# Kernel optimization log

Measured on AMD Instinct MI355X. Metric: run time of the kernel, lower is better.

Reference implementation:

```python
import jax, jax.numpy as jnp
import numpy as np

DIM = 4096
B, S = 4, 2048


def setup_inputs() -> dict:
    key = jax.random.key(0)
    ks = jax.random.split(key, 6)
    scale = 1.0 / np.sqrt(DIM)  # nn.Linear-style init scale
    return {
        "x": jax.random.normal(ks[0], (B, S, DIM), dtype=jnp.float32),
        "W1": jax.random.normal(ks[1], (DIM, DIM), dtype=jnp.float32) * scale,
        "W2": jax.random.normal(ks[2], (DIM, DIM), dtype=jnp.float32) * scale,
        "W3": jax.random.normal(ks[3], (DIM, DIM), dtype=jnp.float32) * scale,
        "W4": jax.random.normal(ks[4], (DIM, DIM), dtype=jnp.float32) * scale,
        "Wo": jax.random.normal(ks[5], (DIM, DIM), dtype=jnp.float32) * scale,
    }


def reference(x, W1, W2, W3, W4, Wo):
    # nn.Linear(bias=False): y = x @ W.T
    xA = jnp.einsum('bsd,ed->bse', x, W1)
    xB = jnp.einsum('bsd,ed->bse', x, W2)
    xC = jnp.einsum('bsd,ed->bse', x, W3)
    # xA^T @ xB over the sequence axis -> [B, dim, dim]
    sq = jnp.einsum('bsd,bse->bde', xA, xB)
    sq = jax.nn.softmax(sq, axis=-1)
    # xC @ sq -> [B, S, dim]
    xO = jnp.einsum('bsd,bde->bse', xC, sq)
    xO = jax.nn.softmax(xO, axis=-1)
    xO = jax.nn.silu(jnp.einsum('bsd,ed->bse', xO, W4))
    return jnp.einsum('bsd,ed->bse', x + xO, Wo)
```

## Files before the change

kernel.cpp:

```cpp
#include <hip/hip_runtime.h>
#include <hip/hip_bf16.h>
#include <stdint.h>

#define DIM 4096
#define NB 4
#define SEQ 2048

typedef __bf16 bf16_t;
typedef __bf16 bf16x8 __attribute__((ext_vector_type(8)));
typedef float f32x4 __attribute__((ext_vector_type(4)));

__device__ __forceinline__ uint16_t f2bf_u(float f) {
  union { float f; uint32_t u; } v; v.f = f;
  uint32_t r = v.u + 0x7FFFu + ((v.u >> 16) & 1u);
  return (uint16_t)(r >> 16);
}

__global__ __launch_bounds__(256) void cvt_f32_bf16_k(const float* __restrict__ in,
                                                      uint16_t* __restrict__ out, long n) {
  long i = ((long)blockIdx.x * 256 + threadIdx.x) * 8;
  long stride = (long)gridDim.x * 256 * 8;
  for (; i < n; i += stride) {
    float4 a = *(const float4*)(in + i);
    float4 b = *(const float4*)(in + i + 4);
    ushort4 o0 = make_ushort4(f2bf_u(a.x), f2bf_u(a.y), f2bf_u(a.z), f2bf_u(a.w));
    ushort4 o1 = make_ushort4(f2bf_u(b.x), f2bf_u(b.y), f2bf_u(b.z), f2bf_u(b.w));
    *(ushort4*)(out + i) = o0;
    *(ushort4*)(out + i + 4) = o1;
  }
}

__device__ __forceinline__ void gload16(const void* g, void* l) {
  __builtin_amdgcn_global_load_lds(
      (const __attribute__((address_space(1))) void*)g,
      (__attribute__((address_space(3))) void*)l,
      16, 0, 0);
}

#define BARX() do { asm volatile("" ::: "memory"); __builtin_amdgcn_s_barrier(); asm volatile("" ::: "memory"); } while (0)
#define VMW(n) asm volatile("s_waitcnt vmcnt(" #n ")" ::: "memory")

__device__ __forceinline__ void readA(bf16x8 (&fa)[4][2], const char* p, int c0, int c1) {
#pragma unroll
  for (int m = 0; m < 4; ++m) {
    fa[m][0] = *(const bf16x8*)(p + m * 2048 + c0);
    fa[m][1] = *(const bf16x8*)(p + m * 2048 + c1);
  }
}
__device__ __forceinline__ void readB(bf16x8 (&fb)[2][2], const char* p, int c0, int c1) {
#pragma unroll
  for (int n = 0; n < 2; ++n) {
    fb[n][0] = *(const bf16x8*)(p + n * 2048 + c0);
    fb[n][1] = *(const bf16x8*)(p + n * 2048 + c1);
  }
}
__device__ __forceinline__ void mmaQ(f32x4 (&acc)[4][2], const bf16x8 (&fa)[4][2],
                                     const bf16x8 (&fb)[2][2]) {
#pragma unroll
  for (int m = 0; m < 4; ++m)
#pragma unroll
    for (int n = 0; n < 2; ++n)
#pragma unroll
      for (int kk = 0; kk < 2; ++kk)
        acc[m][n] = __builtin_amdgcn_mfma_f32_16x16x32_bf16(fa[m][kk], fb[n][kk], acc[m][n], 0, 0, 0);
}
__device__ __forceinline__ void stageH(const bf16_t* gt, int soff, long rsk, char* lb, int t16) {
  gload16(gt + soff, lb + t16);
  gload16(gt + soff + rsk, lb + 8192 + t16);
}

#define PRIO1() __builtin_amdgcn_s_setprio(1)
#define PRIO0() __builtin_amdgcn_s_setprio(0)

template <int EPI>
__global__ __launch_bounds__(512, 2) void gemm256(
    const bf16_t* __restrict__ Abase, const bf16_t* __restrict__ Bbase,
    void* __restrict__ Cout, const float* __restrict__ Xadd,
    int M, int N, int K, long sA, long sB, long sC) {
  __shared__ char smem[131072];
  char* As = smem;
  char* Bs = smem + 65536;

  const int tid = threadIdx.x;
  const int lane = tid & 63;
  const int wave = tid >> 6;
  const int wm = wave >> 2;
  const int wn = wave & 3;
  const int lr = lane & 15;
  const int hi = lane >> 4;

  const int nwg = gridDim.x;
  int wg = blockIdx.x;
  if ((nwg & 7) == 0) wg = (wg & 7) * (nwg >> 3) + (wg >> 3);
  const int nbn = N >> 8;
  const int bm = wg / nbn, bn = wg % nbn;

  const bf16_t* A = Abase + (long)blockIdx.y * sA;
  const bf16_t* B = Bbase + (long)blockIdx.y * sB;
  const bf16_t* A0p = A + (long)(bm * 256) * K;
  const bf16_t* A1p = A0p + (long)128 * K;
  const bf16_t* B0p = B + (long)(bn * 256) * K;
  const bf16_t* B1p = B0p + (long)128 * K;
  const long rsk = (long)64 * K;

  const int t16 = tid * 16;
  const int lp = t16 ^ (((t16 >> 7) & 7) << 4);
  const int soff = (lp >> 7) * K + ((lp & 127) >> 1);

  const int swz = (lr & 7) << 4;
  const int c0 = (hi * 16) ^ swz;
  const int c1 = c0 ^ 64;
  const int aR = (wm * 64 + lr) * 128;
  const int bR = (wn * 32 + lr) * 128;

  f32x4 acc[2][2][4][2] = {};
  bf16x8 fa0[4][2], fa1[4][2], fb0[2][2], fb1[2][2];

  stageH(A0p, soff, rsk, As, t16);
  stageH(A1p, soff, rsk, As + 16384, t16);
  stageH(B0p, soff, rsk, Bs, t16);
  stageH(B1p, soff, rsk, Bs + 16384, t16);
  stageH(A0p + 64, soff, rsk, As + 32768, t16);
  stageH(A1p + 64, soff, rsk, As + 49152, t16);
  stageH(B0p + 64, soff, rsk, Bs + 32768, t16);
  VMW(6);
  BARX();

  const int NIT = K >> 7;
  for (int i = 0; i < NIT; ++i) {
    const bool last = (i == NIT - 1);
    const int k1 = (2 * i + 1) * 64;
    const int k2 = k1 + 64;
    const int k3 = k1 + 128;

    readA(fa0, As + aR, c0, c1);
    readB(fb0, Bs + bR, c0, c1);
    readA(fa1, As + 16384 + aR, c0, c1);
    stageH(B1p + k1, soff, rsk, Bs + 49152, t16);
    PRIO1(); mmaQ(acc[0][0], fa0, fb0); mmaQ(acc[1][0], fa1, fb0); PRIO0();
    VMW(8);
    BARX();
    readB(fb1, Bs + 16384 + bR, c0, c1);
    if (!last) {
      stageH(A0p + k2, soff, rsk, As, t16);
      stageH(A1p + k2, soff, rsk, As + 16384, t16);
      stageH(B0p + k2, soff, rsk, Bs, t16);
    }
    PRIO1(); mmaQ(acc[0][1], fa0, fb1); mmaQ(acc[1][1], fa1, fb1); PRIO0();
    if (last) { VMW(2); } else { VMW(8); }
    BARX();
    readA(fa0, As + 32768 + aR, c0, c1);
    readB(fb0, Bs + 32768 + bR, c0, c1);
    readA(fa1, As + 49152 + aR, c0, c1);
    if (!last) stageH(B1p + k2, soff, rsk, Bs + 16384, t16);
    PRIO1(); mmaQ(acc[0][0], fa0, fb0); mmaQ(acc[1][0], fa1, fb0); PRIO0();
    if (last) { VMW(0); } else { VMW(8); }
    BARX();
    readB(fb1, Bs + 49152 + bR, c0, c1);
    if (!last) {
      stageH(A0p + k3, soff, rsk, As + 32768, t16);
      stageH(A1p + k3, soff, rsk, As + 49152, t16);
      stageH(B0p + k3, soff, rsk, Bs + 32768, t16);
    }
    PRIO1(); mmaQ(acc[0][1], fa0, fb1); mmaQ(acc[1][1], fa1, fb1); PRIO0();
    if (!last) VMW(8);
    BARX();
  }

  const long cb = (long)blockIdx.y * sC;
#pragma unroll
  for (int mh = 0; mh < 2; ++mh)
#pragma unroll
    for (int nh = 0; nh < 2; ++nh)
#pragma unroll
      for (int m = 0; m < 4; ++m)
#pragma unroll
        for (int n = 0; n < 2; ++n)
#pragma unroll
          for (int j = 0; j < 4; ++j) {
            const int row = bm * 256 + mh * 128 + wm * 64 + m * 16 + hi * 4 + j;
            const int col = bn * 256 + nh * 128 + wn * 32 + n * 16 + lr;
            const long idx = cb + (long)row * N + col;
            const float vv = acc[mh][nh][m][n][j];
            if constexpr (EPI == 0) {
              ((uint16_t*)Cout)[idx] = f2bf_u(vv);
            } else if constexpr (EPI == 1) {
              ((float*)Cout)[idx] = vv;
            } else {
              const float sl = vv / (1.f + __expf(-vv));
              ((uint16_t*)Cout)[idx] = f2bf_u(Xadd[idx] + sl);
            }
          }
}

__global__ __launch_bounds__(256) void softmax_row4096(const float* __restrict__ in,
                                                       uint16_t* __restrict__ out) {
  const long row = blockIdx.x;
  const float* r = in + row * 4096;
  const int tid = threadIdx.x;
  float v[16];
#pragma unroll
  for (int i = 0; i < 4; ++i) {
    float4 a = *(const float4*)(r + tid * 16 + i * 4);
    v[i * 4 + 0] = a.x; v[i * 4 + 1] = a.y; v[i * 4 + 2] = a.z; v[i * 4 + 3] = a.w;
  }
  float m = v[0];
#pragma unroll
  for (int j = 1; j < 16; ++j) m = fmaxf(m, v[j]);
#pragma unroll
  for (int o = 32; o; o >>= 1) m = fmaxf(m, __shfl_xor(m, o));
  __shared__ float red[8];
  if ((tid & 63) == 0) red[tid >> 6] = m;
  __syncthreads();
  m = fmaxf(fmaxf(red[0], red[1]), fmaxf(red[2], red[3]));
  float s = 0.f;
#pragma unroll
  for (int j = 0; j < 16; ++j) { v[j] = __expf(v[j] - m); s += v[j]; }
#pragma unroll
  for (int o = 32; o; o >>= 1) s += __shfl_xor(s, o);
  if ((tid & 63) == 0) red[4 + (tid >> 6)] = s;
  __syncthreads();
  s = (red[4] + red[5]) + (red[6] + red[7]);
  float inv = 1.f / s;
#pragma unroll
  for (int i = 0; i < 4; ++i) {
    ushort4 u = make_ushort4(f2bf_u(v[i * 4 + 0] * inv), f2bf_u(v[i * 4 + 1] * inv),
                             f2bf_u(v[i * 4 + 2] * inv), f2bf_u(v[i * 4 + 3] * inv));
    *(ushort4*)(out + row * 4096 + tid * 16 + i * 4) = u;
  }
}

__global__ __launch_bounds__(256) void rowstat4096(const float* __restrict__ in,
                                                   float2* __restrict__ stats) {
  const long row = blockIdx.x;
  const float* r = in + row * 4096;
  const int tid = threadIdx.x;
  float v[16];
#pragma unroll
  for (int i = 0; i < 4; ++i) {
    float4 a = *(const float4*)(r + tid * 16 + i * 4);
    v[i * 4 + 0] = a.x; v[i * 4 + 1] = a.y; v[i * 4 + 2] = a.z; v[i * 4 + 3] = a.w;
  }
  float m = v[0];
#pragma unroll
  for (int j = 1; j < 16; ++j) m = fmaxf(m, v[j]);
#pragma unroll
  for (int o = 32; o; o >>= 1) m = fmaxf(m, __shfl_xor(m, o));
  __shared__ float red[8];
  if ((tid & 63) == 0) red[tid >> 6] = m;
  __syncthreads();
  m = fmaxf(fmaxf(red[0], red[1]), fmaxf(red[2], red[3]));
  float s = 0.f;
#pragma unroll
  for (int j = 0; j < 16; ++j) s += __expf(v[j] - m);
#pragma unroll
  for (int o = 32; o; o >>= 1) s += __shfl_xor(s, o);
  if ((tid & 63) == 0) red[4 + (tid >> 6)] = s;
  __syncthreads();
  if (tid == 0) {
    s = (red[4] + red[5]) + (red[6] + red[7]);
    stats[row] = make_float2(m, 1.f / s);
  }
}

__global__ __launch_bounds__(256) void transposeSM(const float* __restrict__ in,
                                                   const float2* __restrict__ stats,
                                                   uint16_t* __restrict__ out) {
  __shared__ uint16_t t[64][68];
  __shared__ float2 st[64];
  const int tid = threadIdx.x;
  const int bx = blockIdx.x, by = blockIdx.y;
  if (tid < 64) st[tid] = stats[by * 64 + tid];
  __syncthreads();
  const int tr = tid >> 4;
  const int tc4 = (tid & 15) * 4;
#pragma unroll
  for (int i = 0; i < 4; ++i) {
    const int r = tr + i * 16;
    const float2 ms = st[r];
    float4 v = *(const float4*)&in[(long)(by * 64 + r) * 4096 + bx * 64 + tc4];
    t[r][tc4 + 0] = f2bf_u(__expf(v.x - ms.x) * ms.y);
    t[r][tc4 + 1] = f2bf_u(__expf(v.y - ms.x) * ms.y);
    t[r][tc4 + 2] = f2bf_u(__expf(v.z - ms.x) * ms.y);
    t[r][tc4 + 3] = f2bf_u(__expf(v.w - ms.x) * ms.y);
  }
  __syncthreads();
#pragma unroll
  for (int i = 0; i < 4; ++i) {
    const int oc = tr + i * 16;
    ushort4 v = make_ushort4(t[tc4 + 0][oc], t[tc4 + 1][oc], t[tc4 + 2][oc], t[tc4 + 3][oc]);
    *(ushort4*)&out[(long)(bx * 64 + oc) * 4096 + by * 64 + tc4] = v;
  }
}

extern "C" void kernel_launch(void* const* d_in, const int* in_sizes, int n_in,
                              void* d_out, int out_size, void* d_ws, size_t ws_size,
                              hipStream_t stream) {
  const float* x  = (const float*)d_in[0];
  const float* W1 = (const float*)d_in[1];
  const float* W2 = (const float*)d_in[2];
  const float* W3 = (const float*)d_in[3];
  const float* W4 = (const float*)d_in[4];
  const float* Wo = (const float*)d_in[5];

  char* ws = (char*)d_ws;
  const long SD  = (long)SEQ * DIM;
  const long BSD = (long)NB * SD;
  const long DD  = (long)DIM * DIM;

  bf16_t* xbf  = (bf16_t*)(ws + 0L);
  bf16_t* xAT  = (bf16_t*)(ws + 67108864L);
  bf16_t* xBT  = (bf16_t*)(ws + 134217728L);
  void*   R3   = (void*)  (ws + 201326592L);
  bf16_t* Wbf  = (bf16_t*)(ws + 268435456L);
  bf16_t* sqmT = (bf16_t*)(ws + 301989888L);
  float2* stats = (float2*)d_out;
  float*  xOraw = (float*)d_out;
  (void)ws_size; (void)in_sizes; (void)n_in; (void)out_size;

  cvt_f32_bf16_k<<<2048, 256, 0, stream>>>(x, (uint16_t*)xbf, BSD);

  cvt_f32_bf16_k<<<2048, 256, 0, stream>>>(W1, (uint16_t*)Wbf, DD);
  gemm256<0><<<dim3(128, 4), 512, 0, stream>>>(Wbf, xbf, (void*)xAT, nullptr,
                                               DIM, SEQ, DIM, 0, SD, SD);
  cvt_f32_bf16_k<<<2048, 256, 0, stream>>>(W2, (uint16_t*)Wbf, DD);
  gemm256<0><<<dim3(128, 4), 512, 0, stream>>>(Wbf, xbf, (void*)xBT, nullptr,
                                               DIM, SEQ, DIM, 0, SD, SD);

  for (int b = 0; b < NB; ++b) {
    gemm256<1><<<dim3(256, 1), 512, 0, stream>>>(xAT + b * SD, xBT + b * SD, R3, nullptr,
                                                 DIM, DIM, SEQ, 0, 0, 0);
    rowstat4096<<<DIM, 256, 0, stream>>>((const float*)R3, stats);
    transposeSM<<<dim3(64, 64), 256, 0, stream>>>((const float*)R3, stats,
                                                  (uint16_t*)(sqmT + b * DD));
  }

  cvt_f32_bf16_k<<<2048, 256, 0, stream>>>(W3, (uint16_t*)Wbf, DD);
  gemm256<0><<<dim3(512, 1), 512, 0, stream>>>(xbf, Wbf, R3, nullptr,
                                               NB * SEQ, DIM, DIM, 0, 0, 0);

  gemm256<1><<<dim3(128, 4), 512, 0, stream>>>((const bf16_t*)R3, sqmT, (void*)xOraw, nullptr,
                                               SEQ, DIM, DIM, SD, DD, SD);
  softmax_row4096<<<NB * SEQ, 256, 0, stream>>>(xOraw, (uint16_t*)xBT);

  cvt_f32_bf16_k<<<2048, 256, 0, stream>>>(W4, (uint16_t*)Wbf, DD);
  gemm256<2><<<dim3(512, 1), 512, 0, stream>>>(xBT, Wbf, (void*)xbf, x,
                                               NB * SEQ, DIM, DIM, 0, 0, 0);

  cvt_f32_bf16_k<<<2048, 256, 0, stream>>>(Wo, (uint16_t*)Wbf, DD);
  gemm256<1><<<dim3(512, 1), 512, 0, stream>>>(xbf, Wbf, d_out, nullptr,
                                               NB * SEQ, DIM, DIM, 0, 0, 0);
}
```

Before: 1.827 ms.

## Restructure GEMM main loop into eight-stage quadrant pipeline with finer barriers

Reworks the 256x256 bf16 GEMM main loop so that each phase issues one LDS fragment read, one global stage and a single MMA quadrant, separated by barriers. It adds a second B-fragment register set so B0 fragments persist across phases, and peels the final iteration into an epilogue. The aim is to interleave LDS reads, global loads and MFMA work at a finer grain and keep fewer loads in flight per wait. In exchange it doubles the number of barriers and raises register pressure.

```diff
diff --git a/kernel.cpp b/kernel.cpp
--- a/kernel.cpp
+++ b/kernel.cpp
@@ -114,57 +114,81 @@
   const int bR = (wn * 32 + lr) * 128;
 
   f32x4 acc[2][2][4][2] = {};
-  bf16x8 fa0[4][2], fa1[4][2], fb0[2][2], fb1[2][2];
+  bf16x8 fa0[4][2], fa1[4][2], fb0s0[2][2], fb0s1[2][2], fb1[2][2];
 
   stageH(A0p, soff, rsk, As, t16);
+  stageH(B0p, soff, rsk, Bs, t16);
   stageH(A1p, soff, rsk, As + 16384, t16);
-  stageH(B0p, soff, rsk, Bs, t16);
   stageH(B1p, soff, rsk, Bs + 16384, t16);
   stageH(A0p + 64, soff, rsk, As + 32768, t16);
   stageH(A1p + 64, soff, rsk, As + 49152, t16);
-  stageH(B0p + 64, soff, rsk, Bs + 32768, t16);
-  VMW(6);
+  VMW(4);
   BARX();
+  readA(fa0, As + aR, c0, c1);
+  readB(fb0s0, Bs + bR, c0, c1);
 
   const int NIT = K >> 7;
-  for (int i = 0; i < NIT; ++i) {
-    const bool last = (i == NIT - 1);
-    const int k1 = (2 * i + 1) * 64;
-    const int k2 = k1 + 64;
-    const int k3 = k1 + 128;
-
+  for (int i = 0; i < NIT - 1; ++i) {
+    const int kb1 = (2 * i + 1) * 64;
+    const int kb0n = kb1 + 64;
+    const int kb1n = kb1 + 128;
+    readB(fb1, Bs + 16384 + bR, c0, c1);
+    stageH(B0p + kb1, soff, rsk, Bs + 32768, t16);
+    PRIO1(); mmaQ(acc[0][0], fa0, fb0s0); PRIO0();
+    VMW(4); BARX();
+    readA(fa1, As + 16384 + aR, c0, c1);
+    stageH(B1p + kb1, soff, rsk, Bs + 49152, t16);
+    PRIO1(); mmaQ(acc[0][1], fa0, fb1); PRIO0();
+    VMW(4); BARX();
+    readA(fa0, As + 32768 + aR, c0, c1);
+    stageH(A0p + kb0n, soff, rsk, As, t16);
+    PRIO1(); mmaQ(acc[1][1], fa1, fb1); PRIO0();
+    VMW(4); BARX();
+    readB(fb0s1, Bs + 32768 + bR, c0, c1);
+    stageH(A1p + kb0n, soff, rsk, As + 16384, t16);
+    PRIO1(); mmaQ(acc[1][0], fa1, fb0s0); PRIO0();
+    VMW(4); BARX();
+    readB(fb1, Bs + 49152 + bR, c0, c1);
+    stageH(B0p + kb0n, soff, rsk, Bs, t16);
+    PRIO1(); mmaQ(acc[0][0], fa0, fb0s1); PRIO0();
+    VMW(4); BARX();
+    readA(fa1, As + 49152 + aR, c0, c1);
+    stageH(B1p + kb0n, soff, rsk, Bs + 16384, t16);
+    PRIO1(); mmaQ(acc[0][1], fa0, fb1); PRIO0();
+    VMW(4); BARX();
     readA(fa0, As + aR, c0, c1);
-    readB(fb0, Bs + bR, c0, c1);
+    stageH(A0p + kb1n, soff, rsk, As + 32768, t16);
+    PRIO1(); mmaQ(acc[1][1], fa1, fb1); PRIO0();
+    VMW(4); BARX();
+    readB(fb0s0, Bs + bR, c0, c1);
+    stageH(A1p + kb1n, soff, rsk, As + 49152, t16);
+    PRIO1(); mmaQ(acc[1][0], fa1, fb0s1); PRIO0();
+    VMW(4); BARX();
+  }
+  {
+    const int kb1 = (2 * (NIT - 1) + 1) * 64;
+    readB(fb1, Bs + 16384 + bR, c0, c1);
+    stageH(B0p + kb1, soff, rsk, Bs + 32768, t16);
+    PRIO1(); mmaQ(acc[0][0], fa0, fb0s0); PRIO0();
+    VMW(4); BARX();
     readA(fa1, As + 16384 + aR, c0, c1);
-    stageH(B1p + k1, soff, rsk, Bs + 49152, t16);
-    PRIO1(); mmaQ(acc[0][0], fa0, fb0); mmaQ(acc[1][0], fa1, fb0); PRIO0();
-    VMW(8);
+    stageH(B1p + kb1, soff, rsk, Bs + 49152, t16);
+    PRIO1(); mmaQ(acc[0][1], fa0, fb1); PRIO0();
+    VMW(4); BARX();
+    readA(fa0, As + 32768 + aR, c0, c1);
+    PRIO1(); mmaQ(acc[1][1], fa1, fb1); PRIO0();
+    VMW(2); BARX();
+    readB(fb0s1, Bs + 32768 + bR, c0, c1);
+    PRIO1(); mmaQ(acc[1][0], fa1, fb0s0); PRIO0();
+    VMW(0); BARX();
+    readB(fb1, Bs + 49152 + bR, c0, c1);
+    PRIO1(); mmaQ(acc[0][0], fa0, fb0s1); PRIO0();
     BARX();
-    readB(fb1, Bs + 16384 + bR, c0, c1);
-    if (!last) {
-      stageH(A0p + k2, soff, rsk, As, t16);
-      stageH(A1p + k2, soff, rsk, As + 16384, t16);
-      stageH(B0p + k2, soff, rsk, Bs, t16);
-    }
-    PRIO1(); mmaQ(acc[0][1], fa0, fb1); mmaQ(acc[1][1], fa1, fb1); PRIO0();
-    if (last) { VMW(2); } else { VMW(8); }
+    readA(fa1, As + 49152 + aR, c0, c1);
+    PRIO1(); mmaQ(acc[0][1], fa0, fb1); PRIO0();
     BARX();
-    readA(fa0, As + 32768 + aR, c0, c1);
-    readB(fb0, Bs + 32768 + bR, c0, c1);
-    readA(fa1, As + 49152 + aR, c0, c1);
-    if (!last) stageH(B1p + k2, soff, rsk, Bs + 16384, t16);
-    PRIO1(); mmaQ(acc[0][0], fa0, fb0); mmaQ(acc[1][0], fa1, fb0); PRIO0();
-    if (last) { VMW(0); } else { VMW(8); }
-    BARX();
-    readB(fb1, Bs + 49152 + bR, c0, c1);
-    if (!last) {
-      stageH(A0p + k3, soff, rsk, As + 32768, t16);
-      stageH(A1p + k3, soff, rsk, As + 49152, t16);
-      stageH(B0p + k3, soff, rsk, Bs + 32768, t16);
-    }
-    PRIO1(); mmaQ(acc[0][1], fa0, fb1); mmaQ(acc[1][1], fa1, fb1); PRIO0();
-    if (!last) VMW(8);
-    BARX();
+    PRIO1(); mmaQ(acc[1][1], fa1, fb1); PRIO0();
+    PRIO1(); mmaQ(acc[1][0], fa1, fb0s1); PRIO0();
   }
 
   const long cb = (long)blockIdx.y * sC;
```

Result: slower. 3.432 ms (+87.8%).
